# Performance work log

Measured on AMD Instinct MI355X. Metric: run time of the kernel, lower is better.

## Reference

```python
import jax, jax.numpy as jnp
import numpy as np

EMBED_DIM = 1024
NUM_HEADS = 16
DEPTH = EMBED_DIM // NUM_HEADS  # 64
B, S = 4, 2048


def setup_inputs() -> dict:
    key = jax.random.key(0)
    ks = jax.random.split(key, 12)
    sc = 0.02
    return {
        "q": jax.random.normal(ks[0], (B, S, EMBED_DIM), jnp.float32),
        "k": jax.random.normal(ks[1], (B, S, EMBED_DIM), jnp.float32),
        "v": jax.random.normal(ks[2], (B, S, EMBED_DIM), jnp.float32),
        # per-head Dense(depth) weights stacked over heads: [H, D, depth]
        "wq": jax.random.normal(ks[3], (NUM_HEADS, EMBED_DIM, DEPTH), jnp.float32) * sc,
        "bq": jnp.zeros((NUM_HEADS, DEPTH), jnp.float32),
        "wk": jax.random.normal(ks[4], (NUM_HEADS, EMBED_DIM, DEPTH), jnp.float32) * sc,
        "bk": jnp.zeros((NUM_HEADS, DEPTH), jnp.float32),
        "wv": jax.random.normal(ks[5], (NUM_HEADS, EMBED_DIM, DEPTH), jnp.float32) * sc,
        "bv": jnp.zeros((NUM_HEADS, DEPTH), jnp.float32),
        # final Dense(embedding_dim): [D, D]
        "wo": jax.random.normal(ks[6], (EMBED_DIM, EMBED_DIM), jnp.float32) * sc,
        "bo": jnp.zeros((EMBED_DIM,), jnp.float32),
        "use_mask": 1,
    }


def reference(q, k, v, wq, bq, wk, bk, wv, bv, wo, bo, use_mask):
    # Batched per-head projections (equivalent to H separate Dense layers).
    qh = jnp.einsum('bsd,hde->bhse', q, wq) + bq[None, :, None, :]
    kh = jnp.einsum('bsd,hde->bhse', k, wk) + bk[None, :, None, :]
    vh = jnp.einsum('bsd,hde->bhse', v, wv) + bv[None, :, None, :]

    scale = 1.0 / jnp.sqrt(jnp.asarray(DEPTH, jnp.float32))
    logits = jnp.einsum('bhqe,bhke->bhqk', qh, kh) * scale  # [B,H,Sq,Sk]
    if use_mask:
        Sq, Sk = qh.shape[2], kh.shape[2]
        causal = jnp.triu(jnp.ones((Sq, Sk), jnp.float32), k=1)
        logits = logits + causal[None, None, :, :] * (-1e9)
    attn = jax.nn.softmax(logits, axis=-1)
    out_h = jnp.einsum('bhqk,bhke->bhqe', attn, vh)  # [B,H,Sq,depth]
    # concat heads along last dim -> [B,Sq,H*depth]
    bsz, H, Sq, dep = out_h.shape
    concat = out_h.transpose(0, 2, 1, 3).reshape(bsz, Sq, H * dep)
    return concat @ wo + bo
```

## Files before the change

kernel.cpp:

```cpp
#include <hip/hip_runtime.h>

#define B_ 4
#define S_ 2048
#define H_ 16
#define D_ 64
#define E_ 1024
#define M_ 8192

typedef __attribute__((ext_vector_type(8))) __bf16 bf16x8;
typedef __attribute__((ext_vector_type(4))) __bf16 bf16x4;
typedef __attribute__((ext_vector_type(4))) float f32x4;

__device__ __forceinline__ void gload_lds16(const void* g, void* l) {
  __builtin_amdgcn_global_load_lds(
      (const __attribute__((address_space(1))) unsigned int*)g,
      (__attribute__((address_space(3))) unsigned int*)l, 16, 0, 0);
}

__global__ void cvt_f32_bf16(const float* __restrict__ in, __bf16* __restrict__ out) {
  const int i = blockIdx.x * blockDim.x + threadIdx.x;
  const float4 v = ((const float4*)in)[i];
  bf16x4 o;
  o.x = (__bf16)v.x; o.y = (__bf16)v.y; o.z = (__bf16)v.z; o.w = (__bf16)v.w;
  ((bf16x4*)out)[i] = o;
}

__global__ void pack_head_w(const float* __restrict__ w, __bf16* __restrict__ out) {
  const int idx = blockIdx.x * 256 + threadIdx.x;
  const int n = idx >> 10, k = idx & 1023;
  out[idx] = (__bf16)w[((size_t)(n >> 6) << 16) + (k << 6) + (n & 63)];
}
__global__ void pack_wo(const float* __restrict__ w, __bf16* __restrict__ out) {
  const int idx = blockIdx.x * 256 + threadIdx.x;
  const int n = idx >> 10, k = idx & 1023;
  out[idx] = (__bf16)w[((size_t)k << 10) + n];
}

template <int MODE>
__global__ __launch_bounds__(256) void gemm_bt(const __bf16* __restrict__ A,
                                               const __bf16* __restrict__ Bt,
                                               const float* __restrict__ bias,
                                               void* __restrict__ Cout) {
  constexpr int K = 1024;
  __shared__ __bf16 As[128 * 64];
  __shared__ __bf16 Bs[128 * 64];
  const int t = threadIdx.x;
  const int w = t >> 6, l = t & 63;
  const int m0 = blockIdx.x * 128, n0 = blockIdx.y * 128;
  f32x4 acc[4][4] = {};

  for (int kt = 0; kt < K / 64; ++kt) {
    const int kb = kt * 64;
#pragma unroll
    for (int j = 0; j < 4; ++j) {
      const int ci = (j * 4 + w) * 64 + l;
      const int row = ci >> 3;
      const int c = (ci & 7) ^ (row & 7);
      gload_lds16(A + (size_t)(m0 + row) * K + kb + c * 8, As + (j * 4 + w) * 512);
      gload_lds16(Bt + (size_t)(n0 + row) * K + kb + c * 8, Bs + (j * 4 + w) * 512);
    }
    __syncthreads();
#pragma unroll
    for (int kk = 0; kk < 64; kk += 32) {
      bf16x8 af[4], bfr[4];
#pragma unroll
      for (int f = 0; f < 4; ++f) {
        const int ra = (w >> 1) * 64 + f * 16 + (l & 15);
        const int ca = ((kk >> 3) + (l >> 4)) ^ (ra & 7);
        af[f] = *(const bf16x8*)(As + ra * 64 + ca * 8);
        const int rb = (w & 1) * 64 + f * 16 + (l & 15);
        const int cb = ((kk >> 3) + (l >> 4)) ^ (rb & 7);
        bfr[f] = *(const bf16x8*)(Bs + rb * 64 + cb * 8);
      }
#pragma unroll
      for (int mf = 0; mf < 4; ++mf)
#pragma unroll
        for (int nf = 0; nf < 4; ++nf)
          acc[mf][nf] = __builtin_amdgcn_mfma_f32_16x16x32_bf16(af[mf], bfr[nf],
                                                                acc[mf][nf], 0, 0, 0);
    }
    __syncthreads();
  }

#pragma unroll
  for (int mf = 0; mf < 4; ++mf) {
#pragma unroll
    for (int nf = 0; nf < 4; ++nf) {
#pragma unroll
      for (int r = 0; r < 4; ++r) {
        const int gm = m0 + (w >> 1) * 64 + mf * 16 + (l >> 4) * 4 + r;
        const int gn = n0 + (w & 1) * 64 + nf * 16 + (l & 15);
        const float val = acc[mf][nf][r] + ((MODE == 1) ? bias[gm] : bias[gn]);
        if constexpr (MODE == 0) {
          ((__bf16*)Cout)[(((size_t)(gm >> 11) * H_ + (gn >> 6)) * S_ + (gm & 2047)) * D_ + (gn & 63)] =
              (__bf16)val;
        } else if constexpr (MODE == 1) {
          ((__bf16*)Cout)[(((size_t)(gn >> 11) * H_ + (gm >> 6)) * D_ + (gm & 63)) * S_ + (gn & 2047)] =
              (__bf16)val;
        } else {
          ((float*)Cout)[(size_t)gm * 1024 + gn] = val;
        }
      }
    }
  }
}

__global__ __launch_bounds__(512) void attn_fused(const __bf16* __restrict__ qh,
                                                  const __bf16* __restrict__ kh,
                                                  const __bf16* __restrict__ vT,
                                                  __bf16* __restrict__ concat,
                                                  const int* __restrict__ use_mask_p) {
  __shared__ __bf16 Ks[2][64 * 64];
  __shared__ __bf16 Vs[2][64 * 64];
  __shared__ __bf16 Pl[8][16 * 72];
  const int t = threadIdx.x, w = t >> 6, l = t & 63;
  const int pair = blockIdx.x, bh = blockIdx.y;
  const int usemask = *use_mask_p;
  const __bf16* Qb = qh + (size_t)bh * S_ * D_;
  const __bf16* Kb = kh + (size_t)bh * S_ * D_;
  const __bf16* Vb = vT + (size_t)bh * D_ * S_;
  const int b = bh >> 4, hh = bh & 15;
  constexpr float LOG2E = 1.4426950408889634f;

  const int srow = t >> 3;
  const int sc = (t & 7) ^ (srow & 7);

  bf16x8 ones;
#pragma unroll
  for (int i = 0; i < 8; ++i) ones[i] = (__bf16)1.0f;

  __bf16* Pw = &Pl[w][0];
  int cur = 0;

  for (int half = 0; half < 2; ++half) {
    const int qt = half ? (15 - pair) : pair;
    const int qrow0 = qt * 128 + w * 16;
    const int ktend = usemask ? (2 * qt + 1) : (S_ / 64 - 1);

    bf16x8 qf[2];
#pragma unroll
    for (int kf = 0; kf < 2; ++kf)
      qf[kf] = *(const bf16x8*)(Qb + (size_t)(qrow0 + (l & 15)) * D_ + kf * 32 + (l >> 4) * 8);

    float mrow[4] = {-3e38f, -3e38f, -3e38f, -3e38f};
    f32x4 ls = {};
    f32x4 o[4] = {};

    gload_lds16(Kb + (size_t)(0 * 64 + srow) * D_ + sc * 8, &Ks[cur][w * 512]);
    gload_lds16(Vb + (size_t)srow * S_ + 0 * 64 + sc * 8, &Vs[cur][w * 512]);
    __builtin_amdgcn_sched_barrier(0);
    asm volatile("s_waitcnt vmcnt(0)" ::: "memory");
    __builtin_amdgcn_s_barrier();
    __builtin_amdgcn_sched_barrier(0);

    for (int kt = 0; kt <= ktend; ++kt) {
      if (kt < ktend) {
        const int nxt = cur ^ 1;
        gload_lds16(Kb + (size_t)((kt + 1) * 64 + srow) * D_ + sc * 8, &Ks[nxt][w * 512]);
        gload_lds16(Vb + (size_t)srow * S_ + (kt + 1) * 64 + sc * 8, &Vs[nxt][w * 512]);
      }

      f32x4 s[4] = {};
      __builtin_amdgcn_s_setprio(1);
#pragma unroll
      for (int kf = 0; kf < 2; ++kf) {
        bf16x8 kfrag[4];
#pragma unroll
        for (int nf = 0; nf < 4; ++nf) {
          const int row = nf * 16 + (l & 15);
          const int c = (kf * 4 + (l >> 4)) ^ (row & 7);
          kfrag[nf] = *(const bf16x8*)(&Ks[cur][row * 64 + c * 8]);
        }
#pragma unroll
        for (int nf = 0; nf < 4; ++nf)
          s[nf] = __builtin_amdgcn_mfma_f32_16x16x32_bf16(qf[kf], kfrag[nf], s[nf], 0, 0, 0);
      }
      __builtin_amdgcn_s_setprio(0);
#pragma unroll
      for (int nf = 0; nf < 4; ++nf) s[nf] *= 0.125f;

      if (usemask && kt * 64 + 63 > qrow0) {
#pragma unroll
        for (int nf = 0; nf < 4; ++nf) {
          const int col = kt * 64 + nf * 16 + (l & 15);
#pragma unroll
          for (int r = 0; r < 4; ++r) {
            const int rq = qrow0 + (l >> 4) * 4 + r;
            if (col > rq) s[nf][r] = -1e30f;
          }
        }
      }

      float pm[4];
#pragma unroll
      for (int r = 0; r < 4; ++r)
        pm[r] = fmaxf(fmaxf(s[0][r], s[1][r]), fmaxf(s[2][r], s[3][r]));
#pragma unroll
      for (int off = 1; off < 16; off <<= 1)
#pragma unroll
        for (int r = 0; r < 4; ++r) pm[r] = fmaxf(pm[r], __shfl_xor(pm[r], off));

      const int skip = __all((pm[0] - mrow[0] <= 8.0f) && (pm[1] - mrow[1] <= 8.0f) &&
                             (pm[2] - mrow[2] <= 8.0f) && (pm[3] - mrow[3] <= 8.0f));
      if (!skip) {
        float al[4];
#pragma unroll
        for (int r = 0; r < 4; ++r) {
          const float mn = fmaxf(mrow[r], pm[r]);
          al[r] = __builtin_amdgcn_exp2f((mrow[r] - mn) * LOG2E);
          mrow[r] = mn;
          ls[r] *= al[r];
        }
#pragma unroll
        for (int nf = 0; nf < 4; ++nf)
#pragma unroll
          for (int r = 0; r < 4; ++r) o[nf][r] *= al[r];
      }

#pragma unroll
      for (int nf = 0; nf < 4; ++nf)
#pragma unroll
        for (int r = 0; r < 4; ++r)
          Pw[((l >> 4) * 4 + r) * 72 + nf * 16 + (l & 15)] =
              (__bf16)__builtin_amdgcn_exp2f((s[nf][r] - mrow[r]) * LOG2E);

      __builtin_amdgcn_s_setprio(1);
#pragma unroll
      for (int kk = 0; kk < 2; ++kk) {
        const bf16x8 pa = *(const bf16x8*)(Pw + (l & 15) * 72 + kk * 32 + (l >> 4) * 8);
        bf16x8 vf[4];
#pragma unroll
        for (int nf = 0; nf < 4; ++nf) {
          const int row = nf * 16 + (l & 15);
          const int c = (kk * 4 + (l >> 4)) ^ (row & 7);
          vf[nf] = *(const bf16x8*)(&Vs[cur][row * 64 + c * 8]);
        }
#pragma unroll
        for (int nf = 0; nf < 4; ++nf)
          o[nf] = __builtin_amdgcn_mfma_f32_16x16x32_bf16(pa, vf[nf], o[nf], 0, 0, 0);
        ls = __builtin_amdgcn_mfma_f32_16x16x32_bf16(pa, ones, ls, 0, 0, 0);
      }
      __builtin_amdgcn_s_setprio(0);

      __builtin_amdgcn_sched_barrier(0);
      asm volatile("s_waitcnt vmcnt(0)" ::: "memory");
      __builtin_amdgcn_s_barrier();
      __builtin_amdgcn_sched_barrier(0);
      cur ^= 1;
    }

#pragma unroll
    for (int r = 0; r < 4; ++r) {
      const float inv = 1.0f / ls[r];
      const int qr = qrow0 + (l >> 4) * 4 + r;
#pragma unroll
      for (int nf = 0; nf < 4; ++nf)
        concat[((size_t)(b * S_ + qr)) * E_ + hh * 64 + nf * 16 + (l & 15)] =
            (__bf16)(o[nf][r] * inv);
    }
  }
}

extern "C" void kernel_launch(void* const* d_in, const int* in_sizes, int n_in,
                              void* d_out, int out_size, void* d_ws, size_t ws_size,
                              hipStream_t stream) {
  const float* q = (const float*)d_in[0];
  const float* k = (const float*)d_in[1];
  const float* v = (const float*)d_in[2];
  const float* wq = (const float*)d_in[3];
  const float* bq = (const float*)d_in[4];
  const float* wk = (const float*)d_in[5];
  const float* bk = (const float*)d_in[6];
  const float* wv = (const float*)d_in[7];
  const float* bv = (const float*)d_in[8];
  const float* wo = (const float*)d_in[9];
  const float* bo = (const float*)d_in[10];
  const int* use_mask = (const int*)d_in[11];
  (void)in_sizes; (void)n_in; (void)out_size; (void)ws_size;

  char* ws = (char*)d_ws;
  __bf16* Aq = (__bf16*)ws;
  __bf16* Ak = Aq + (size_t)M_ * E_;
  __bf16* Av = Ak + (size_t)M_ * E_;
  __bf16* Bq = Av + (size_t)M_ * E_;
  __bf16* Bk = Bq + (size_t)E_ * E_;
  __bf16* Bv = Bk + (size_t)E_ * E_;
  __bf16* Bo = Bv + (size_t)E_ * E_;
  __bf16* qhb = Bo + (size_t)E_ * E_;
  __bf16* khb = qhb + (size_t)8388608;
  __bf16* vTb = khb + (size_t)8388608;
  __bf16* concat = Aq;

  cvt_f32_bf16<<<8192, 256, 0, stream>>>(q, Aq);
  cvt_f32_bf16<<<8192, 256, 0, stream>>>(k, Ak);
  cvt_f32_bf16<<<8192, 256, 0, stream>>>(v, Av);
  pack_head_w<<<4096, 256, 0, stream>>>(wq, Bq);
  pack_head_w<<<4096, 256, 0, stream>>>(wk, Bk);
  pack_head_w<<<4096, 256, 0, stream>>>(wv, Bv);
  pack_wo<<<4096, 256, 0, stream>>>(wo, Bo);
  gemm_bt<0><<<dim3(64, 8), 256, 0, stream>>>(Aq, Bq, bq, qhb);
  gemm_bt<0><<<dim3(64, 8), 256, 0, stream>>>(Ak, Bk, bk, khb);
  gemm_bt<1><<<dim3(8, 64), 256, 0, stream>>>(Bv, Av, bv, vTb);
  attn_fused<<<dim3(8, 64), 512, 0, stream>>>(qhb, khb, vTb, concat, use_mask);
  gemm_bt<2><<<dim3(64, 8), 256, 0, stream>>>(concat, Bo, bo, d_out);
}
```

Before: 238.2 us.

## Rewrite attention with 32x32 MFMA, transposed S, register-resident P via permlane

```diff
diff --git a/kernel.cpp b/kernel.cpp
--- a/kernel.cpp
+++ b/kernel.cpp
@@ -10,11 +10,18 @@
 typedef __attribute__((ext_vector_type(8))) __bf16 bf16x8;
 typedef __attribute__((ext_vector_type(4))) __bf16 bf16x4;
 typedef __attribute__((ext_vector_type(4))) float f32x4;
+typedef __attribute__((ext_vector_type(16))) float f32x16;
 
 __device__ __forceinline__ void gload_lds16(const void* g, void* l) {
   __builtin_amdgcn_global_load_lds(
       (const __attribute__((address_space(1))) unsigned int*)g,
       (__attribute__((address_space(3))) unsigned int*)l, 16, 0, 0);
+}
+
+__device__ __forceinline__ unsigned pk2(float a, float b) {
+  union { __bf16 h; unsigned short u; } ua, ub;
+  ua.h = (__bf16)a; ub.h = (__bf16)b;
+  return ((unsigned)ub.u << 16) | (unsigned)ua.u;
 }
 
 __global__ void cvt_f32_bf16(const float* __restrict__ in, __bf16* __restrict__ out) {
@@ -105,158 +112,164 @@
   }
 }
 
-__global__ __launch_bounds__(512) void attn_fused(const __bf16* __restrict__ qh,
-                                                  const __bf16* __restrict__ kh,
-                                                  const __bf16* __restrict__ vT,
-                                                  __bf16* __restrict__ concat,
-                                                  const int* __restrict__ use_mask_p) {
+__global__ __launch_bounds__(512, 2) void attn_fused(const __bf16* __restrict__ qh,
+                                                     const __bf16* __restrict__ kh,
+                                                     const __bf16* __restrict__ vT,
+                                                     __bf16* __restrict__ concat,
+                                                     const int* __restrict__ use_mask_p) {
   __shared__ __bf16 Ks[2][64 * 64];
   __shared__ __bf16 Vs[2][64 * 64];
-  __shared__ __bf16 Pl[8][16 * 72];
   const int t = threadIdx.x, w = t >> 6, l = t & 63;
-  const int pair = blockIdx.x, bh = blockIdx.y;
+  const int lo = l & 31, hi = l >> 5;
+  const int bh = blockIdx.x, pair = blockIdx.y;
   const int usemask = *use_mask_p;
   const __bf16* Qb = qh + (size_t)bh * S_ * D_;
   const __bf16* Kb = kh + (size_t)bh * S_ * D_;
   const __bf16* Vb = vT + (size_t)bh * D_ * S_;
   const int b = bh >> 4, hh = bh & 15;
-  constexpr float LOG2E = 1.4426950408889634f;
+  constexpr float CEXP = 0.125f * 1.4426950408889634f;
 
   const int srow = t >> 3;
   const int sc = (t & 7) ^ (srow & 7);
 
-  bf16x8 ones;
-#pragma unroll
-  for (int i = 0; i < 8; ++i) ones[i] = (__bf16)1.0f;
-
-  __bf16* Pw = &Pl[w][0];
   int cur = 0;
-
   for (int half = 0; half < 2; ++half) {
-    const int qt = half ? (15 - pair) : pair;
-    const int qrow0 = qt * 128 + w * 16;
-    const int ktend = usemask ? (2 * qt + 1) : (S_ / 64 - 1);
-
-    bf16x8 qf[2];
-#pragma unroll
-    for (int kf = 0; kf < 2; ++kf)
-      qf[kf] = *(const bf16x8*)(Qb + (size_t)(qrow0 + (l & 15)) * D_ + kf * 32 + (l >> 4) * 8);
-
-    float mrow[4] = {-3e38f, -3e38f, -3e38f, -3e38f};
-    f32x4 ls = {};
-    f32x4 o[4] = {};
-
-    gload_lds16(Kb + (size_t)(0 * 64 + srow) * D_ + sc * 8, &Ks[cur][w * 512]);
-    gload_lds16(Vb + (size_t)srow * S_ + 0 * 64 + sc * 8, &Vs[cur][w * 512]);
-    __builtin_amdgcn_sched_barrier(0);
-    asm volatile("s_waitcnt vmcnt(0)" ::: "memory");
-    __builtin_amdgcn_s_barrier();
-    __builtin_amdgcn_sched_barrier(0);
-
-    for (int kt = 0; kt <= ktend; ++kt) {
-      if (kt < ktend) {
-        const int nxt = cur ^ 1;
-        gload_lds16(Kb + (size_t)((kt + 1) * 64 + srow) * D_ + sc * 8, &Ks[nxt][w * 512]);
-        gload_lds16(Vb + (size_t)srow * S_ + (kt + 1) * 64 + sc * 8, &Vs[nxt][w * 512]);
-      }
-
-      f32x4 s[4] = {};
-      __builtin_amdgcn_s_setprio(1);
-#pragma unroll
-      for (int kf = 0; kf < 2; ++kf) {
-        bf16x8 kfrag[4];
-#pragma unroll
-        for (int nf = 0; nf < 4; ++nf) {
-          const int row = nf * 16 + (l & 15);
-          const int c = (kf * 4 + (l >> 4)) ^ (row & 7);
-          kfrag[nf] = *(const bf16x8*)(&Ks[cur][row * 64 + c * 8]);
-        }
-#pragma unroll
-        for (int nf = 0; nf < 4; ++nf)
-          s[nf] = __builtin_amdgcn_mfma_f32_16x16x32_bf16(qf[kf], kfrag[nf], s[nf], 0, 0, 0);
-      }
-      __builtin_amdgcn_s_setprio(0);
-#pragma unroll
-      for (int nf = 0; nf < 4; ++nf) s[nf] *= 0.125f;
-
-      if (usemask && kt * 64 + 63 > qrow0) {
-#pragma unroll
-        for (int nf = 0; nf < 4; ++nf) {
-          const int col = kt * 64 + nf * 16 + (l & 15);
-#pragma unroll
-          for (int r = 0; r < 4; ++r) {
-            const int rq = qrow0 + (l >> 4) * 4 + r;
-            if (col > rq) s[nf][r] = -1e30f;
-          }
-        }
-      }
-
-      float pm[4];
-#pragma unroll
-      for (int r = 0; r < 4; ++r)
-        pm[r] = fmaxf(fmaxf(s[0][r], s[1][r]), fmaxf(s[2][r], s[3][r]));
-#pragma unroll
-      for (int off = 1; off < 16; off <<= 1)
-#pragma unroll
-        for (int r = 0; r < 4; ++r) pm[r] = fmaxf(pm[r], __shfl_xor(pm[r], off));
-
-      const int skip = __all((pm[0] - mrow[0] <= 8.0f) && (pm[1] - mrow[1] <= 8.0f) &&
-                             (pm[2] - mrow[2] <= 8.0f) && (pm[3] - mrow[3] <= 8.0f));
-      if (!skip) {
-        float al[4];
-#pragma unroll
-        for (int r = 0; r < 4; ++r) {
-          const float mn = fmaxf(mrow[r], pm[r]);
-          al[r] = __builtin_amdgcn_exp2f((mrow[r] - mn) * LOG2E);
-          mrow[r] = mn;
-          ls[r] *= al[r];
-        }
-#pragma unroll
-        for (int nf = 0; nf < 4; ++nf)
-#pragma unroll
-          for (int r = 0; r < 4; ++r) o[nf][r] *= al[r];
-      }
-
-#pragma unroll
-      for (int nf = 0; nf < 4; ++nf)
-#pragma unroll
-        for (int r = 0; r < 4; ++r)
-          Pw[((l >> 4) * 4 + r) * 72 + nf * 16 + (l & 15)] =
-              (__bf16)__builtin_amdgcn_exp2f((s[nf][r] - mrow[r]) * LOG2E);
-
-      __builtin_amdgcn_s_setprio(1);
-#pragma unroll
-      for (int kk = 0; kk < 2; ++kk) {
-        const bf16x8 pa = *(const bf16x8*)(Pw + (l & 15) * 72 + kk * 32 + (l >> 4) * 8);
-        bf16x8 vf[4];
-#pragma unroll
-        for (int nf = 0; nf < 4; ++nf) {
-          const int row = nf * 16 + (l & 15);
-          const int c = (kk * 4 + (l >> 4)) ^ (row & 7);
-          vf[nf] = *(const bf16x8*)(&Vs[cur][row * 64 + c * 8]);
-        }
-#pragma unroll
-        for (int nf = 0; nf < 4; ++nf)
-          o[nf] = __builtin_amdgcn_mfma_f32_16x16x32_bf16(pa, vf[nf], o[nf], 0, 0, 0);
-        ls = __builtin_amdgcn_mfma_f32_16x16x32_bf16(pa, ones, ls, 0, 0, 0);
-      }
-      __builtin_amdgcn_s_setprio(0);
-
+    const int qt = half ? (7 - pair) : pair;
+    const int qrow0 = qt * 256 + w * 32;
+    const int nkt = usemask ? (4 * qt + 4) : (S_ / 64);
+    const int ktw = usemask ? (4 * qt + (w >> 1)) : 100000;
+    const int ktdiag = usemask ? (4 * qt + (w >> 1)) : -1;
+
+    bf16x8 qf[4];
+#pragma unroll
+    for (int ks = 0; ks < 4; ++ks)
+      qf[ks] = *(const bf16x8*)(Qb + (size_t)(qrow0 + lo) * D_ + ks * 16 + hi * 8);
+
+    float m = -3e38f, ls = 0.f;
+    f32x16 o0 = {}, o1 = {};
+
+    gload_lds16(Kb + (size_t)(0 + srow) * D_ + sc * 8, &Ks[cur][w * 512]);
+    gload_lds16(Vb + (size_t)srow * S_ + 0 + sc * 8, &Vs[cur][w * 512]);
+
+    for (int kt = 0; kt < nkt; ++kt) {
       __builtin_amdgcn_sched_barrier(0);
       asm volatile("s_waitcnt vmcnt(0)" ::: "memory");
       __builtin_amdgcn_s_barrier();
       __builtin_amdgcn_sched_barrier(0);
+
+      if (kt + 1 < nkt) {
+        const int nxt = cur ^ 1;
+        gload_lds16(Kb + (size_t)((kt + 1) * 64 + srow) * D_ + sc * 8, &Ks[nxt][w * 512]);
+        gload_lds16(Vb + (size_t)srow * S_ + (kt + 1) * 64 + sc * 8, &Vs[nxt][w * 512]);
+      }
+
+      if (kt <= ktw) {
+        f32x16 s0 = {}, s1 = {};
+        __builtin_amdgcn_s_setprio(1);
+#pragma unroll
+        for (int ks = 0; ks < 4; ++ks) {
+          const int ch = ((ks << 1) | hi) ^ (lo & 7);
+          const bf16x8 k0 = *(const bf16x8*)(&Ks[cur][lo * 64 + ch * 8]);
+          const bf16x8 k1 = *(const bf16x8*)(&Ks[cur][(32 + lo) * 64 + ch * 8]);
+          s0 = __builtin_amdgcn_mfma_f32_32x32x16_bf16(k0, qf[ks], s0, 0, 0, 0);
+          s1 = __builtin_amdgcn_mfma_f32_32x32x16_bf16(k1, qf[ks], s1, 0, 0, 0);
+        }
+        __builtin_amdgcn_s_setprio(0);
+
+        if (kt == ktdiag) {
+          const int qloc = ((w & 1) << 5) + lo;
+#pragma unroll
+          for (int r = 0; r < 16; ++r) {
+            const int kv0 = (r & 3) + 8 * (r >> 2) + 4 * hi;
+            if (kv0 > qloc) s0[r] = -1e30f;
+            if (kv0 + 32 > qloc) s1[r] = -1e30f;
+          }
+        }
+
+        float pm = s0[0];
+#pragma unroll
+        for (int r = 1; r < 16; ++r) pm = fmaxf(pm, s0[r]);
+#pragma unroll
+        for (int r = 0; r < 16; ++r) pm = fmaxf(pm, s1[r]);
+        pm = fmaxf(pm, __shfl_xor(pm, 32));
+
+        if (!__all(pm - m <= 64.0f)) {
+          const float mn = fmaxf(m, pm);
+          const float al = __builtin_amdgcn_exp2f((m - mn) * CEXP);
+          m = mn;
+          ls *= al;
+          o0 *= al;
+          o1 *= al;
+        }
+
+        unsigned W0[4][2], W1[4][2];
+        float rs0 = 0.f, rs1 = 0.f;
+#pragma unroll
+        for (int j = 0; j < 4; ++j) {
+          float p0 = __builtin_amdgcn_exp2f((s0[4 * j + 0] - m) * CEXP);
+          float p1 = __builtin_amdgcn_exp2f((s0[4 * j + 1] - m) * CEXP);
+          float p2 = __builtin_amdgcn_exp2f((s0[4 * j + 2] - m) * CEXP);
+          float p3 = __builtin_amdgcn_exp2f((s0[4 * j + 3] - m) * CEXP);
+          rs0 += (p0 + p1) + (p2 + p3);
+          W0[j][0] = pk2(p0, p1);
+          W0[j][1] = pk2(p2, p3);
+          float q0 = __builtin_amdgcn_exp2f((s1[4 * j + 0] - m) * CEXP);
+          float q1 = __builtin_amdgcn_exp2f((s1[4 * j + 1] - m) * CEXP);
+          float q2 = __builtin_amdgcn_exp2f((s1[4 * j + 2] - m) * CEXP);
+          float q3 = __builtin_amdgcn_exp2f((s1[4 * j + 3] - m) * CEXP);
+          rs1 += (q0 + q1) + (q2 + q3);
+          W1[j][0] = pk2(q0, q1);
+          W1[j][1] = pk2(q2, q3);
+        }
+        float rs = rs0 + rs1;
+        rs += __shfl_xor(rs, 32);
+        ls += rs;
+
+        bf16x8 pa[4];
+#pragma unroll
+        for (int ks = 0; ks < 4; ++ks) {
+          const int c = ks & 1;
+          unsigned x0, x1, y0, y1;
+          if ((ks >> 1) == 0) {
+            x0 = W0[2 * c][0]; x1 = W0[2 * c][1];
+            y0 = W0[2 * c + 1][0]; y1 = W0[2 * c + 1][1];
+          } else {
+            x0 = W1[2 * c][0]; x1 = W1[2 * c][1];
+            y0 = W1[2 * c + 1][0]; y1 = W1[2 * c + 1][1];
+          }
+          asm volatile("v_permlane32_swap_b32 %0, %1" : "+v"(x0), "+v"(y0));
+          asm volatile("v_permlane32_swap_b32 %0, %1" : "+v"(x1), "+v"(y1));
+          union { unsigned u[4]; bf16x8 v; } uu;
+          uu.u[0] = x0; uu.u[1] = x1; uu.u[2] = y0; uu.u[3] = y1;
+          pa[ks] = uu.v;
+        }
+
+        __builtin_amdgcn_s_setprio(1);
+#pragma unroll
+        for (int ks = 0; ks < 4; ++ks) {
+          const int ch = ((ks << 1) | hi) ^ (lo & 7);
+          const bf16x8 v0 = *(const bf16x8*)(&Vs[cur][lo * 64 + ch * 8]);
+          const bf16x8 v1 = *(const bf16x8*)(&Vs[cur][(32 + lo) * 64 + ch * 8]);
+          o0 = __builtin_amdgcn_mfma_f32_32x32x16_bf16(v0, pa[ks], o0, 0, 0, 0);
+          o1 = __builtin_amdgcn_mfma_f32_32x32x16_bf16(v1, pa[ks], o1, 0, 0, 0);
+        }
+        __builtin_amdgcn_s_setprio(0);
+      }
       cur ^= 1;
     }
 
-#pragma unroll
-    for (int r = 0; r < 4; ++r) {
-      const float inv = 1.0f / ls[r];
-      const int qr = qrow0 + (l >> 4) * 4 + r;
-#pragma unroll
-      for (int nf = 0; nf < 4; ++nf)
-        concat[((size_t)(b * S_ + qr)) * E_ + hh * 64 + nf * 16 + (l & 15)] =
-            (__bf16)(o[nf][r] * inv);
+    const float inv = 1.0f / ls;
+    const size_t rowbase = ((size_t)(b * S_ + qrow0 + lo)) * E_ + hh * 64;
+#pragma unroll
+    for (int rr = 0; rr < 4; ++rr) {
+      bf16x4 v0, v1;
+#pragma unroll
+      for (int bb = 0; bb < 4; ++bb) {
+        v0[bb] = (__bf16)(o0[4 * rr + bb] * inv);
+        v1[bb] = (__bf16)(o1[4 * rr + bb] * inv);
+      }
+      *(bf16x4*)(concat + rowbase + 8 * rr + 4 * hi) = v0;
+      *(bf16x4*)(concat + rowbase + 32 + 8 * rr + 4 * hi) = v1;
     }
   }
 }
@@ -301,6 +314,6 @@
   gemm_bt<0><<<dim3(64, 8), 256, 0, stream>>>(Aq, Bq, bq, qhb);
   gemm_bt<0><<<dim3(64, 8), 256, 0, stream>>>(Ak, Bk, bk, khb);
   gemm_bt<1><<<dim3(8, 64), 256, 0, stream>>>(Bv, Av, bv, vTb);
-  attn_fused<<<dim3(8, 64), 512, 0, stream>>>(qhb, khb, vTb, concat, use_mask);
+  attn_fused<<<dim3(64, 4), 512, 0, stream>>>(qhb, khb, vTb, concat, use_mask);
   gemm_bt<2><<<dim3(64, 8), 256, 0, stream>>>(concat, Bo, bo, d_out);
 }
```

Measured after the change: 216.1 us. -9.3%, faster.
